# Kernel tuning notes

Hardware: AMD Instinct MI355X
Metric: run time of the kernel (lower is better)

The kernel has to match this reference:

```python
import jax, jax.numpy as jnp
import numpy as np

B = 256
D = 512
C = 100000
S = 30.0
M = 0.5
COS_M = float(np.cos(M))
SIN_M = float(np.sin(M))
TH = float(np.cos(np.pi - M))
MM = float(np.sin(np.pi - M) * M)


def setup_inputs() -> dict:
    key = jax.random.key(0)
    k1, k2, k3, k4 = jax.random.split(key, 4)
    image_emb = jax.random.normal(k1, (B, D), dtype=jnp.float32)
    profile_emb = jax.random.normal(k2, (B, D), dtype=jnp.float32)
    # xavier_uniform_ for weight [C, D]: bound = sqrt(6/(C+D))
    bound = float(np.sqrt(6.0 / (C + D)))
    weight = jax.random.uniform(k3, (C, D), dtype=jnp.float32, minval=-bound, maxval=bound)
    label = jax.random.randint(k4, (B,), 0, C, dtype=jnp.int64)
    return {"image_emb": image_emb, "profile_emb": profile_emb, "weight": weight, "label": label}


def reference(image_emb, profile_emb, weight, label):
    emb = jnp.concatenate([image_emb, profile_emb], axis=0)          # [2B, D]
    lab = jnp.tile(label, (2,))                                      # [2B]
    emb_n = emb / jnp.linalg.norm(emb, axis=1, keepdims=True)
    w_n = weight / jnp.linalg.norm(weight, axis=1, keepdims=True)
    cosine = jnp.einsum('nd,cd->nc', emb_n, w_n)                     # [2B, C]
    sine = jnp.sqrt(jnp.clip(1.0 - cosine * cosine, 0.0, 1.0))
    phi = cosine * COS_M - sine * SIN_M
    phi = jnp.where(cosine > TH, phi, cosine - MM)                   # easy_margin=False
    one_hot = jnp.arange(cosine.shape[1])[None, :] == lab[:, None]   # [2B, C] bool
    logits = S * jnp.where(one_hot, phi, cosine)
    logp = jax.nn.log_softmax(logits, axis=1)
    nll = -jnp.take_along_axis(logp, lab[:, None], axis=1)[:, 0]
    return jnp.mean(nll)
```

## Files before the change

### kernel.cpp

```cpp
#include <hip/hip_runtime.h>

#define S_SCALE 30.0f
#define COS_M 0.8775825618903728f
#define SIN_M 0.479425538604203f
#define TH_C (-0.8775825618903728f)
#define MM_C 0.2397127693021015f

#define BD 512
#define DD 512
#define CC 100000
#define NCB2 782
#define LASTB2 781
#define NPART 1564

typedef __bf16 bf16x8 __attribute__((ext_vector_type(8)));
typedef float  f32x4  __attribute__((ext_vector_type(4)));

#define AS1 __attribute__((address_space(1)))
#define AS3 __attribute__((address_space(3)))

__global__ __launch_bounds__(256) void k_prep(const float* __restrict__ img,
                                              const float* __restrict__ prof,
                                              const float* __restrict__ W,
                                              const int* __restrict__ lab,
                                              __bf16* __restrict__ At,
                                              float* __restrict__ sphi,
                                              float* __restrict__ scos) {
    const int t = threadIdx.x;
    const int wave = t >> 6, l = t & 63;
    const int row = blockIdx.x * 4 + wave;
    const float* src = (row < 256) ? (img + (size_t)row * DD) : (prof + (size_t)(row - 256) * DD);
    float4 v0 = ((const float4*)src)[l * 2];
    float4 v1 = ((const float4*)src)[l * 2 + 1];
    float s = v0.x * v0.x + v0.y * v0.y + v0.z * v0.z + v0.w * v0.w
            + v1.x * v1.x + v1.y * v1.y + v1.z * v1.z + v1.w * v1.w;
    #pragma unroll
    for (int o = 1; o < 64; o <<= 1) s += __shfl_xor(s, o);
    float r = rsqrtf(s);
    bf16x8 a;
    a[0] = (__bf16)(v0.x * r); a[1] = (__bf16)(v0.y * r);
    a[2] = (__bf16)(v0.z * r); a[3] = (__bf16)(v0.w * r);
    a[4] = (__bf16)(v1.x * r); a[5] = (__bf16)(v1.y * r);
    a[6] = (__bf16)(v1.z * r); a[7] = (__bf16)(v1.w * r);
    *(bf16x8*)(At + (size_t)(l >> 2) * (BD * 32) + row * 32 + (l & 3) * 8) = a;

    const int c = lab[row & 255];
    const float4* wc = (const float4*)(W + (size_t)c * DD);
    float4 w0 = wc[l * 2], w1 = wc[l * 2 + 1];
    float wb0 = (float)(__bf16)w0.x, wb1 = (float)(__bf16)w0.y;
    float wb2 = (float)(__bf16)w0.z, wb3 = (float)(__bf16)w0.w;
    float wb4 = (float)(__bf16)w1.x, wb5 = (float)(__bf16)w1.y;
    float wb6 = (float)(__bf16)w1.z, wb7 = (float)(__bf16)w1.w;
    float dot = (float)a[0] * wb0 + (float)a[1] * wb1 + (float)a[2] * wb2 + (float)a[3] * wb3
              + (float)a[4] * wb4 + (float)a[5] * wb5 + (float)a[6] * wb6 + (float)a[7] * wb7;
    float wsq = wb0 * wb0 + wb1 * wb1 + wb2 * wb2 + wb3 * wb3
              + wb4 * wb4 + wb5 * wb5 + wb6 * wb6 + wb7 * wb7;
    #pragma unroll
    for (int o = 1; o < 64; o <<= 1) { dot += __shfl_xor(dot, o); wsq += __shfl_xor(wsq, o); }
    if (l == 0) {
        float cs = dot * rsqrtf(wsq);
        float sn = sqrtf(fmaxf(0.f, fminf(1.f, 1.f - cs * cs)));
        float phi = cs * COS_M - sn * SIN_M;
        if (!(cs > TH_C)) phi = cs - MM_C;
        sphi[row] = S_SCALE * phi;
        scos[row] = S_SCALE * cs;
    }
}

__global__ __launch_bounds__(256, 3) void k_gemm(const __bf16* __restrict__ At,
                                                 const float* __restrict__ W,
                                                 float* __restrict__ part) {
    __shared__ __bf16 As[2][128 * 32];
    __shared__ __bf16 Bs[2][128 * 32];

    const int t = threadIdx.x;
    const int bid = blockIdx.x;
    const int swz = (bid & 7) * 391 + (bid >> 3);
    const int rb = swz & 3;
    const int cb = swz >> 2;
    const int wave = t >> 6, lane = t & 63, q = lane >> 4, m16 = lane & 15;
    const int wr = wave >> 1, wc = wave & 1;

    const int frag_off = m16 * 32 + ((q ^ ((m16 >> 1) & 3)) << 3);

    const int wcol = t >> 1, h = t & 1;
    const int gc = cb * 128 + wcol;
    const float* wp = W + (size_t)(gc < CC ? gc : 0) * DD + h * 16;
    const int bofs0 = wcol * 32 + (((h * 2 + 0) ^ ((wcol >> 1) & 3)) << 3);
    const int bofs1 = wcol * 32 + (((h * 2 + 1) ^ ((wcol >> 1) & 3)) << 3);

    const int srcswz = ((t >> 2) << 6) + ((((t & 3) ^ ((t >> 3) & 3))) << 4);
    const char* abase = (const char*)At + (size_t)rb * 8192 + srcswz;

    f32x4 acc[4][4] = {};
    float sq = 0.f;
    float4 wr0, wr1, wr2, wr3;
    bf16x8 nb0, nb1;

#define GLDS_TILE(kt, buf)                                                              \
    {                                                                                   \
        _Pragma("unroll")                                                               \
        for (int rr = 0; rr < 2; ++rr) {                                                \
            __builtin_amdgcn_global_load_lds(                                           \
                (AS1 void*)(abase + (size_t)(kt) * 32768 + rr * 4096),                  \
                (AS3 void*)((char*)(&As[buf][0]) + rr * 4096 + wave * 1024),            \
                16, 0, 0);                                                              \
        }                                                                               \
    }

#define LOADW(n)                                                                        \
    {                                                                                   \
        wr0 = *(const float4*)(wp + (n) * 32);                                          \
        wr1 = *(const float4*)(wp + (n) * 32 + 4);                                      \
        wr2 = *(const float4*)(wp + (n) * 32 + 8);                                      \
        wr3 = *(const float4*)(wp + (n) * 32 + 12);                                     \
    }

#define CVTW()                                                                          \
    {                                                                                   \
        nb0[0] = (__bf16)wr0.x; nb0[1] = (__bf16)wr0.y;                                 \
        nb0[2] = (__bf16)wr0.z; nb0[3] = (__bf16)wr0.w;                                 \
        nb0[4] = (__bf16)wr1.x; nb0[5] = (__bf16)wr1.y;                                 \
        nb0[6] = (__bf16)wr1.z; nb0[7] = (__bf16)wr1.w;                                 \
        nb1[0] = (__bf16)wr2.x; nb1[1] = (__bf16)wr2.y;                                 \
        nb1[2] = (__bf16)wr2.z; nb1[3] = (__bf16)wr2.w;                                 \
        nb1[4] = (__bf16)wr3.x; nb1[5] = (__bf16)wr3.y;                                 \
        nb1[6] = (__bf16)wr3.z; nb1[7] = (__bf16)wr3.w;                                 \
        float f;                                                                        \
        f = (float)nb0[0]; sq += f * f; f = (float)nb0[1]; sq += f * f;                 \
        f = (float)nb0[2]; sq += f * f; f = (float)nb0[3]; sq += f * f;                 \
        f = (float)nb0[4]; sq += f * f; f = (float)nb0[5]; sq += f * f;                 \
        f = (float)nb0[6]; sq += f * f; f = (float)nb0[7]; sq += f * f;                 \
        f = (float)nb1[0]; sq += f * f; f = (float)nb1[1]; sq += f * f;                 \
        f = (float)nb1[2]; sq += f * f; f = (float)nb1[3]; sq += f * f;                 \
        f = (float)nb1[4]; sq += f * f; f = (float)nb1[5]; sq += f * f;                 \
        f = (float)nb1[6]; sq += f * f; f = (float)nb1[7]; sq += f * f;                 \
    }

#define WRITEBS(buf)                                                                    \
    {                                                                                   \
        *(bf16x8*)(&Bs[buf][bofs0]) = nb0;                                              \
        *(bf16x8*)(&Bs[buf][bofs1]) = nb1;                                              \
    }

    GLDS_TILE(0, 0);
    LOADW(0);
    CVTW();
    WRITEBS(0);
    LOADW(1);

    #pragma unroll
    for (int kt = 0; kt < 16; ++kt) {
        __syncthreads();
        if (kt < 15) {
            GLDS_TILE(kt + 1, (kt + 1) & 1);
            CVTW();
            WRITEBS((kt + 1) & 1);
        }
        if (kt < 14) LOADW(kt + 2);

        bf16x8 bfrag[4], afrag[4];
        #pragma unroll
        for (int j = 0; j < 4; ++j)
            bfrag[j] = *(const bf16x8*)(&Bs[kt & 1][wc * 2048 + j * 512 + frag_off]);
        #pragma unroll
        for (int i = 0; i < 4; ++i)
            afrag[i] = *(const bf16x8*)(&As[kt & 1][wr * 2048 + i * 512 + frag_off]);
        #pragma unroll
        for (int i = 0; i < 4; ++i) {
            #pragma unroll
            for (int j = 0; j < 4; ++j)
                acc[i][j] = __builtin_amdgcn_mfma_f32_16x16x32_bf16(
                    afrag[i], bfrag[j], acc[i][j], 0, 0, 0);
        }
    }

    __syncthreads();
    float* csq = (float*)&As[0][0];
    sq += __shfl_xor(sq, 1);
    if (h == 0) csq[wcol] = sq;
    __syncthreads();

    const bool lastb = (cb == LASTB2);
    float inv[4]; bool val[4];
    #pragma unroll
    for (int j = 0; j < 4; ++j) {
        int ct = wc * 64 + j * 16 + m16;
        val[j] = (!lastb) || (ct < 32);
        inv[j] = rsqrtf(csq[ct]) * S_SCALE;
    }
    #pragma unroll
    for (int i = 0; i < 4; ++i) {
        #pragma unroll
        for (int r = 0; r < 4; ++r) {
            float e = 0.f;
            #pragma unroll
            for (int j = 0; j < 4; ++j)
                if (val[j]) e += __expf(acc[i][j][r] * inv[j]);
            e += __shfl_xor(e, 1);
            e += __shfl_xor(e, 2);
            e += __shfl_xor(e, 4);
            e += __shfl_xor(e, 8);
            if (m16 == 0)
                part[((size_t)cb * 2 + wc) * BD + rb * 128 + wr * 64 + i * 16 + q * 4 + r] = e;
        }
    }
#undef GLDS_TILE
#undef LOADW
#undef CVTW
#undef WRITEBS
}

__global__ __launch_bounds__(256) void k_reduce1(const float* __restrict__ part,
                                                 float* __restrict__ rowpart) {
    const int b = blockIdx.x;
    const int rg = b >> 5, cp = b & 31;
    const int t = threadIdx.x;
    const int rl = t & 63, ph = t >> 6;
    const int r0 = rg * 64;
    float s = 0.f;
    for (int c0 = cp * 4 + ph; c0 < NPART; c0 += 128)
        s += part[(size_t)c0 * BD + r0 + rl];
    __shared__ float buf[256];
    buf[t] = s;
    __syncthreads();
    if (t < 64)
        rowpart[(size_t)cp * BD + r0 + t] = buf[t] + buf[t + 64] + buf[t + 128] + buf[t + 192];
}

__global__ __launch_bounds__(256) void k_final(const float* __restrict__ rowpart,
                                               const float* __restrict__ sphi,
                                               const float* __restrict__ scos,
                                               float* __restrict__ out) {
    const int t = threadIdx.x;
    float a = 0.f;
    for (int r = t; r < BD; r += 256) {
        float total = 0.f;
        #pragma unroll
        for (int cp = 0; cp < 32; ++cp)
            total += rowpart[(size_t)cp * BD + r];
        float lse = logf(total);
        float sp = sphi[r], sc = scos[r];
        float corr = log1pf(__expf(sp - lse) - __expf(sc - lse));
        a += lse + corr - sp;
    }
    for (int o = 1; o < 64; o <<= 1) a += __shfl_xor(a, o);
    __shared__ float wsum[4];
    if ((t & 63) == 0) wsum[t >> 6] = a;
    __syncthreads();
    if (t == 0) out[0] = (wsum[0] + wsum[1] + wsum[2] + wsum[3]) * (1.0f / 512.0f);
}

extern "C" void kernel_launch(void* const* d_in, const int* in_sizes, int n_in,
                              void* d_out, int out_size, void* d_ws, size_t ws_size,
                              hipStream_t stream) {
    const float* img  = (const float*)d_in[0];
    const float* prof = (const float*)d_in[1];
    const float* W    = (const float*)d_in[2];
    const int*   lab  = (const int*)d_in[3];

    char* ws = (char*)d_ws;
    __bf16* At     = (__bf16*)ws;
    float* sphi    = (float*)(ws + 524288);
    float* scos    = (float*)(ws + 526336);
    float* part    = (float*)(ws + 528384);
    float* rowpart = (float*)(ws + 3731456);

    k_prep<<<128, 256, 0, stream>>>(img, prof, W, lab, At, sphi, scos);
    k_gemm<<<4 * NCB2, 256, 0, stream>>>(At, W, part);
    k_reduce1<<<256, 256, 0, stream>>>(part, rowpart);
    k_final<<<1, 256, 0, stream>>>(rowpart, sphi, scos, (float*)d_out);
}
```

Measured before the change: 357.2 us.

## Pre-convert weights to tiled bf16 in prep kernel and fuse final reduction

The prep kernel now also converts the full fp32 weight matrix into a pre-swizzled bf16 tiled buffer and precomputes per-class squared norms. The GEMM can then load B tiles with direct global-to-LDS loads instead of loading fp32, converting in registers and writing to LDS four times over (once per row block). The final reduction is folded into the reduce kernel using an atomic last-block counter, removing one launch. In exchange, the full weight matrix is read in fp32 and written back in bf16 on every call, which adds traffic before the GEMM starts.

```diff
diff --git a/kernel.cpp b/kernel.cpp
--- a/kernel.cpp
+++ b/kernel.cpp
@@ -12,8 +12,10 @@
 #define NCB2 782
 #define LASTB2 781
 #define NPART 1564
+#define CPAD 100096
 
 typedef __bf16 bf16x8 __attribute__((ext_vector_type(8)));
+typedef __bf16 bf16x4 __attribute__((ext_vector_type(4)));
 typedef float  f32x4  __attribute__((ext_vector_type(4)));
 
 #define AS1 __attribute__((address_space(1)))
@@ -25,50 +27,92 @@
                                               const int* __restrict__ lab,
                                               __bf16* __restrict__ At,
                                               float* __restrict__ sphi,
-                                              float* __restrict__ scos) {
+                                              float* __restrict__ scos,
+                                              __bf16* __restrict__ Wt,
+                                              float* __restrict__ csqg,
+                                              int* __restrict__ cnt) {
     const int t = threadIdx.x;
     const int wave = t >> 6, l = t & 63;
-    const int row = blockIdx.x * 4 + wave;
-    const float* src = (row < 256) ? (img + (size_t)row * DD) : (prof + (size_t)(row - 256) * DD);
-    float4 v0 = ((const float4*)src)[l * 2];
-    float4 v1 = ((const float4*)src)[l * 2 + 1];
-    float s = v0.x * v0.x + v0.y * v0.y + v0.z * v0.z + v0.w * v0.w
-            + v1.x * v1.x + v1.y * v1.y + v1.z * v1.z + v1.w * v1.w;
-    #pragma unroll
-    for (int o = 1; o < 64; o <<= 1) s += __shfl_xor(s, o);
-    float r = rsqrtf(s);
-    bf16x8 a;
-    a[0] = (__bf16)(v0.x * r); a[1] = (__bf16)(v0.y * r);
-    a[2] = (__bf16)(v0.z * r); a[3] = (__bf16)(v0.w * r);
-    a[4] = (__bf16)(v1.x * r); a[5] = (__bf16)(v1.y * r);
-    a[6] = (__bf16)(v1.z * r); a[7] = (__bf16)(v1.w * r);
-    *(bf16x8*)(At + (size_t)(l >> 2) * (BD * 32) + row * 32 + (l & 3) * 8) = a;
-
-    const int c = lab[row & 255];
-    const float4* wc = (const float4*)(W + (size_t)c * DD);
-    float4 w0 = wc[l * 2], w1 = wc[l * 2 + 1];
-    float wb0 = (float)(__bf16)w0.x, wb1 = (float)(__bf16)w0.y;
-    float wb2 = (float)(__bf16)w0.z, wb3 = (float)(__bf16)w0.w;
-    float wb4 = (float)(__bf16)w1.x, wb5 = (float)(__bf16)w1.y;
-    float wb6 = (float)(__bf16)w1.z, wb7 = (float)(__bf16)w1.w;
-    float dot = (float)a[0] * wb0 + (float)a[1] * wb1 + (float)a[2] * wb2 + (float)a[3] * wb3
-              + (float)a[4] * wb4 + (float)a[5] * wb5 + (float)a[6] * wb6 + (float)a[7] * wb7;
-    float wsq = wb0 * wb0 + wb1 * wb1 + wb2 * wb2 + wb3 * wb3
-              + wb4 * wb4 + wb5 * wb5 + wb6 * wb6 + wb7 * wb7;
-    #pragma unroll
-    for (int o = 1; o < 64; o <<= 1) { dot += __shfl_xor(dot, o); wsq += __shfl_xor(wsq, o); }
-    if (l == 0) {
-        float cs = dot * rsqrtf(wsq);
-        float sn = sqrtf(fmaxf(0.f, fminf(1.f, 1.f - cs * cs)));
-        float phi = cs * COS_M - sn * SIN_M;
-        if (!(cs > TH_C)) phi = cs - MM_C;
-        sphi[row] = S_SCALE * phi;
-        scos[row] = S_SCALE * cs;
+
+    if (blockIdx.x < 128) {
+        if (blockIdx.x == 0 && t == 0) cnt[0] = 0;
+        const int row = blockIdx.x * 4 + wave;
+        const float* src = (row < 256) ? (img + (size_t)row * DD)
+                                       : (prof + (size_t)(row - 256) * DD);
+        float4 v0 = ((const float4*)src)[l * 2];
+        float4 v1 = ((const float4*)src)[l * 2 + 1];
+        float s = v0.x * v0.x + v0.y * v0.y + v0.z * v0.z + v0.w * v0.w
+                + v1.x * v1.x + v1.y * v1.y + v1.z * v1.z + v1.w * v1.w;
+        #pragma unroll
+        for (int o = 1; o < 64; o <<= 1) s += __shfl_xor(s, o);
+        float r = rsqrtf(s);
+        bf16x8 a;
+        a[0] = (__bf16)(v0.x * r); a[1] = (__bf16)(v0.y * r);
+        a[2] = (__bf16)(v0.z * r); a[3] = (__bf16)(v0.w * r);
+        a[4] = (__bf16)(v1.x * r); a[5] = (__bf16)(v1.y * r);
+        a[6] = (__bf16)(v1.z * r); a[7] = (__bf16)(v1.w * r);
+        *(bf16x8*)(At + (size_t)(l >> 2) * (BD * 32) + row * 32 + (l & 3) * 8) = a;
+
+        const int c = lab[row & 255];
+        const float4* wc = (const float4*)(W + (size_t)c * DD);
+        float4 w0 = wc[l * 2], w1 = wc[l * 2 + 1];
+        float wb0 = (float)(__bf16)w0.x, wb1 = (float)(__bf16)w0.y;
+        float wb2 = (float)(__bf16)w0.z, wb3 = (float)(__bf16)w0.w;
+        float wb4 = (float)(__bf16)w1.x, wb5 = (float)(__bf16)w1.y;
+        float wb6 = (float)(__bf16)w1.z, wb7 = (float)(__bf16)w1.w;
+        float dot = (float)a[0] * wb0 + (float)a[1] * wb1 + (float)a[2] * wb2
+                  + (float)a[3] * wb3 + (float)a[4] * wb4 + (float)a[5] * wb5
+                  + (float)a[6] * wb6 + (float)a[7] * wb7;
+        float wsq = wb0 * wb0 + wb1 * wb1 + wb2 * wb2 + wb3 * wb3
+                  + wb4 * wb4 + wb5 * wb5 + wb6 * wb6 + wb7 * wb7;
+        #pragma unroll
+        for (int o = 1; o < 64; o <<= 1) { dot += __shfl_xor(dot, o); wsq += __shfl_xor(wsq, o); }
+        if (l == 0) {
+            float cs = dot * rsqrtf(wsq);
+            float sn = sqrtf(fmaxf(0.f, fminf(1.f, 1.f - cs * cs)));
+            float phi = cs * COS_M - sn * SIN_M;
+            if (!(cs > TH_C)) phi = cs - MM_C;
+            sphi[row] = S_SCALE * phi;
+            scos[row] = S_SCALE * cs;
+        }
+        return;
+    }
+
+    const int cb = blockIdx.x - 128;
+    char* wtb = (char*)Wt + (size_t)cb * 16 * 8192;
+    for (int p = 0; p < 32; ++p) {
+        const int c  = wave * 32 + p;
+        const int gc = cb * 128 + c;
+        bf16x4 b0, b1;
+        float sq = 0.f;
+        if (gc < CC) {
+            const float4* src = (const float4*)(W + (size_t)gc * DD);
+            float4 f0 = src[l];
+            float4 f1 = src[64 + l];
+            b0[0] = (__bf16)f0.x; b0[1] = (__bf16)f0.y;
+            b0[2] = (__bf16)f0.z; b0[3] = (__bf16)f0.w;
+            b1[0] = (__bf16)f1.x; b1[1] = (__bf16)f1.y;
+            b1[2] = (__bf16)f1.z; b1[3] = (__bf16)f1.w;
+            float f;
+            f = (float)b0[0]; sq += f * f; f = (float)b0[1]; sq += f * f;
+            f = (float)b0[2]; sq += f * f; f = (float)b0[3]; sq += f * f;
+            f = (float)b1[0]; sq += f * f; f = (float)b1[1]; sq += f * f;
+            f = (float)b1[2]; sq += f * f; f = (float)b1[3]; sq += f * f;
+        } else {
+            b0 = bf16x4{(__bf16)0.f, (__bf16)0.f, (__bf16)0.f, (__bf16)0.f};
+            b1 = b0;
+        }
+        #pragma unroll
+        for (int o = 1; o < 64; o <<= 1) sq += __shfl_xor(sq, o);
+        *(bf16x4*)(wtb + (size_t)(l >> 3) * 8192 + c * 64 + (l & 7) * 8) = b0;
+        *(bf16x4*)(wtb + (size_t)(8 + (l >> 3)) * 8192 + c * 64 + (l & 7) * 8) = b1;
+        if (l == 0) csqg[gc] = sq;
     }
 }
 
 __global__ __launch_bounds__(256, 3) void k_gemm(const __bf16* __restrict__ At,
-                                                 const float* __restrict__ W,
+                                                 const __bf16* __restrict__ Wt,
+                                                 const float* __restrict__ csqg,
                                                  float* __restrict__ part) {
     __shared__ __bf16 As[2][128 * 32];
     __shared__ __bf16 Bs[2][128 * 32];
@@ -82,83 +126,42 @@
     const int wr = wave >> 1, wc = wave & 1;
 
     const int frag_off = m16 * 32 + ((q ^ ((m16 >> 1) & 3)) << 3);
-
-    const int wcol = t >> 1, h = t & 1;
-    const int gc = cb * 128 + wcol;
-    const float* wp = W + (size_t)(gc < CC ? gc : 0) * DD + h * 16;
-    const int bofs0 = wcol * 32 + (((h * 2 + 0) ^ ((wcol >> 1) & 3)) << 3);
-    const int bofs1 = wcol * 32 + (((h * 2 + 1) ^ ((wcol >> 1) & 3)) << 3);
-
-    const int srcswz = ((t >> 2) << 6) + ((((t & 3) ^ ((t >> 3) & 3))) << 4);
+    const int srcswz   = ((t >> 2) << 6) + ((((t & 3) ^ ((t >> 3) & 3))) << 4);
+
     const char* abase = (const char*)At + (size_t)rb * 8192 + srcswz;
+    const char* bbase = (const char*)Wt + (size_t)cb * 131072 + srcswz;
 
     f32x4 acc[4][4] = {};
-    float sq = 0.f;
-    float4 wr0, wr1, wr2, wr3;
-    bf16x8 nb0, nb1;
-
-#define GLDS_TILE(kt, buf)                                                              \
+
+#define GLDS_A(kt, buf)                                                                 \
     {                                                                                   \
         _Pragma("unroll")                                                               \
-        for (int rr = 0; rr < 2; ++rr) {                                                \
+        for (int rr = 0; rr < 2; ++rr)                                                  \
             __builtin_amdgcn_global_load_lds(                                           \
                 (AS1 void*)(abase + (size_t)(kt) * 32768 + rr * 4096),                  \
                 (AS3 void*)((char*)(&As[buf][0]) + rr * 4096 + wave * 1024),            \
                 16, 0, 0);                                                              \
-        }                                                                               \
-    }
-
-#define LOADW(n)                                                                        \
+    }
+#define GLDS_B(kt, buf)                                                                 \
     {                                                                                   \
-        wr0 = *(const float4*)(wp + (n) * 32);                                          \
-        wr1 = *(const float4*)(wp + (n) * 32 + 4);                                      \
-        wr2 = *(const float4*)(wp + (n) * 32 + 8);                                      \
-        wr3 = *(const float4*)(wp + (n) * 32 + 12);                                     \
-    }
-
-#define CVTW()                                                                          \
-    {                                                                                   \
-        nb0[0] = (__bf16)wr0.x; nb0[1] = (__bf16)wr0.y;                                 \
-        nb0[2] = (__bf16)wr0.z; nb0[3] = (__bf16)wr0.w;                                 \
-        nb0[4] = (__bf16)wr1.x; nb0[5] = (__bf16)wr1.y;                                 \
-        nb0[6] = (__bf16)wr1.z; nb0[7] = (__bf16)wr1.w;                                 \
-        nb1[0] = (__bf16)wr2.x; nb1[1] = (__bf16)wr2.y;                                 \
-        nb1[2] = (__bf16)wr2.z; nb1[3] = (__bf16)wr2.w;                                 \
-        nb1[4] = (__bf16)wr3.x; nb1[5] = (__bf16)wr3.y;                                 \
-        nb1[6] = (__bf16)wr3.z; nb1[7] = (__bf16)wr3.w;                                 \
-        float f;                                                                        \
-        f = (float)nb0[0]; sq += f * f; f = (float)nb0[1]; sq += f * f;                 \
-        f = (float)nb0[2]; sq += f * f; f = (float)nb0[3]; sq += f * f;                 \
-        f = (float)nb0[4]; sq += f * f; f = (float)nb0[5]; sq += f * f;                 \
-        f = (float)nb0[6]; sq += f * f; f = (float)nb0[7]; sq += f * f;                 \
-        f = (float)nb1[0]; sq += f * f; f = (float)nb1[1]; sq += f * f;                 \
-        f = (float)nb1[2]; sq += f * f; f = (float)nb1[3]; sq += f * f;                 \
-        f = (float)nb1[4]; sq += f * f; f = (float)nb1[5]; sq += f * f;                 \
-        f = (float)nb1[6]; sq += f * f; f = (float)nb1[7]; sq += f * f;                 \
-    }
-
-#define WRITEBS(buf)                                                                    \
-    {                                                                                   \
-        *(bf16x8*)(&Bs[buf][bofs0]) = nb0;                                              \
-        *(bf16x8*)(&Bs[buf][bofs1]) = nb1;                                              \
-    }
-
-    GLDS_TILE(0, 0);
-    LOADW(0);
-    CVTW();
-    WRITEBS(0);
-    LOADW(1);
+        _Pragma("unroll")                                                               \
+        for (int rr = 0; rr < 2; ++rr)                                                  \
+            __builtin_amdgcn_global_load_lds(                                           \
+                (AS1 void*)(bbase + (size_t)(kt) * 8192 + rr * 4096),                   \
+                (AS3 void*)((char*)(&Bs[buf][0]) + rr * 4096 + wave * 1024),            \
+                16, 0, 0);                                                              \
+    }
+
+    GLDS_A(0, 0);
+    GLDS_B(0, 0);
 
     #pragma unroll
     for (int kt = 0; kt < 16; ++kt) {
         __syncthreads();
         if (kt < 15) {
-            GLDS_TILE(kt + 1, (kt + 1) & 1);
-            CVTW();
-            WRITEBS((kt + 1) & 1);
-        }
-        if (kt < 14) LOADW(kt + 2);
-
+            GLDS_A(kt + 1, (kt + 1) & 1);
+            GLDS_B(kt + 1, (kt + 1) & 1);
+        }
         bf16x8 bfrag[4], afrag[4];
         #pragma unroll
         for (int j = 0; j < 4; ++j)
@@ -175,19 +178,13 @@
         }
     }
 
-    __syncthreads();
-    float* csq = (float*)&As[0][0];
-    sq += __shfl_xor(sq, 1);
-    if (h == 0) csq[wcol] = sq;
-    __syncthreads();
-
     const bool lastb = (cb == LASTB2);
     float inv[4]; bool val[4];
     #pragma unroll
     for (int j = 0; j < 4; ++j) {
         int ct = wc * 64 + j * 16 + m16;
         val[j] = (!lastb) || (ct < 32);
-        inv[j] = rsqrtf(csq[ct]) * S_SCALE;
+        inv[j] = rsqrtf(csqg[cb * 128 + ct]) * S_SCALE;
     }
     #pragma unroll
     for (int i = 0; i < 4; ++i) {
@@ -205,14 +202,16 @@
                 part[((size_t)cb * 2 + wc) * BD + rb * 128 + wr * 64 + i * 16 + q * 4 + r] = e;
         }
     }
-#undef GLDS_TILE
-#undef LOADW
-#undef CVTW
-#undef WRITEBS
-}
-
-__global__ __launch_bounds__(256) void k_reduce1(const float* __restrict__ part,
-                                                 float* __restrict__ rowpart) {
+#undef GLDS_A
+#undef GLDS_B
+}
+
+__global__ __launch_bounds__(256) void k_reduce(const float* __restrict__ part,
+                                                const float* __restrict__ sphi,
+                                                const float* __restrict__ scos,
+                                                float* __restrict__ rowpart,
+                                                int* __restrict__ cnt,
+                                                float* __restrict__ out) {
     const int b = blockIdx.x;
     const int rg = b >> 5, cp = b & 31;
     const int t = threadIdx.x;
@@ -226,24 +225,27 @@
     __syncthreads();
     if (t < 64)
         rowpart[(size_t)cp * BD + r0 + t] = buf[t] + buf[t + 64] + buf[t + 128] + buf[t + 192];
-}
-
-__global__ __launch_bounds__(256) void k_final(const float* __restrict__ rowpart,
-                                               const float* __restrict__ sphi,
-                                               const float* __restrict__ scos,
-                                               float* __restrict__ out) {
-    const int t = threadIdx.x;
+
+    __threadfence();
+    __syncthreads();
+    __shared__ int lastf;
+    if (t == 0) lastf = (atomicAdd(cnt, 1) == 255) ? 1 : 0;
+    __syncthreads();
+    if (!lastf) return;
+    __threadfence();
+
     float a = 0.f;
     for (int r = t; r < BD; r += 256) {
         float total = 0.f;
         #pragma unroll
-        for (int cp = 0; cp < 32; ++cp)
-            total += rowpart[(size_t)cp * BD + r];
+        for (int c = 0; c < 32; ++c)
+            total += rowpart[(size_t)c * BD + r];
         float lse = logf(total);
         float sp = sphi[r], sc = scos[r];
         float corr = log1pf(__expf(sp - lse) - __expf(sc - lse));
         a += lse + corr - sp;
     }
+    #pragma unroll
     for (int o = 1; o < 64; o <<= 1) a += __shfl_xor(a, o);
     __shared__ float wsum[4];
     if ((t & 63) == 0) wsum[t >> 6] = a;
@@ -265,9 +267,11 @@
     float* scos    = (float*)(ws + 526336);
     float* part    = (float*)(ws + 528384);
     float* rowpart = (float*)(ws + 3731456);
-
-    k_prep<<<128, 256, 0, stream>>>(img, prof, W, lab, At, sphi, scos);
-    k_gemm<<<4 * NCB2, 256, 0, stream>>>(At, W, part);
-    k_reduce1<<<256, 256, 0, stream>>>(part, rowpart);
-    k_final<<<1, 256, 0, stream>>>(rowpart, sphi, scos, (float*)d_out);
-}
+    float* csqg    = (float*)(ws + 3796992);
+    int*   cnt     = (int*)(ws + 4197376);
+    __bf16* Wt     = (__bf16*)(ws + 4198400);
+
+    k_prep<<<910, 256, 0, stream>>>(img, prof, W, lab, At, sphi, scos, Wt, csqg, cnt);
+    k_gemm<<<4 * NCB2, 256, 0, stream>>>(At, Wt, csqg, part);
+    k_reduce<<<256, 256, 0, stream>>>(part, sphi, scos, rowpart, cnt, (float*)d_out);
+}
```

Measured after the change: 426.7 us. 1.19x slower.
